# Kernel tuning notes

Measured on AMD Instinct MI355X. Metric: run time of the kernel, lower is better.

## Reference

```python
import jax, jax.numpy as jnp
import numpy as np

# Model dims
B, S, H, NH = 2, 2048, 1024, 8
HD = H // NH            # head_dim = 128
T = S * NH              # MoE input tokens per batch = 16384
E, K, F = 8, 2, 512     # experts, top_k, expert FFN dim (4*head_dim)


def setup_inputs() -> dict:
    key = jax.random.key(0)
    ks = jax.random.split(key, 9)
    s = 0.02  # init scale
    return {
        "x": jax.random.normal(ks[0], (B, S, H), jnp.float32),
        "W_mh": jax.random.normal(ks[1], (H, H), jnp.float32) * s,
        "b_mh": jnp.zeros((H,), jnp.float32),
        "W_merge": jax.random.normal(ks[2], (H, H), jnp.float32) * s,
        "b_merge": jnp.zeros((H,), jnp.float32),
        "W_router": jax.random.normal(ks[3], (HD, E), jnp.float32) * s,
        "W1": jax.random.normal(ks[4], (E, HD, F), jnp.float32) * s,
        "b1": jnp.zeros((E, F), jnp.float32),
        "W2": jax.random.normal(ks[5], (E, F, HD), jnp.float32) * s,
        "b2": jnp.zeros((E, HD), jnp.float32),
    }


def reference(x, W_mh, b_mh, W_merge, b_merge, W_router, W1, b1, W2, b2):
    # multi-head projection then split heads into the token axis
    h = x @ W_mh + b_mh                       # [B, S, H]
    h = h.reshape(B, T, HD)                   # [B, T, HD]

    # nested VectorizedMoE: top-k token-choice routing over head_dim tokens
    logits = h @ W_router                     # [B, T, E]
    probs = jax.nn.softmax(logits, axis=-1)
    topv, topi = jax.lax.top_k(probs, K)      # [B, T, K]
    topv = topv / jnp.sum(topv, axis=-1, keepdims=True)  # renormalize top-k gates
    # scatter top-k gates into dense [B, T, E] combine weights
    gates = jnp.sum(jax.nn.one_hot(topi, E, dtype=h.dtype) * topv[..., None], axis=-2)

    # vectorized expert FFNs (all experts, combined with sparse gates)
    a = jax.nn.gelu(jnp.einsum('btd,edf->btef', h, W1) + b1)   # [B, T, E, F]
    y = jnp.einsum('btef,efd->bted', a, W2) + b2               # [B, T, E, HD]
    moe_out = jnp.einsum('bte,bted->btd', gates, y)            # [B, T, HD]

    # merge heads back and final projection
    out = moe_out.reshape(B, S, H) @ W_merge + b_merge         # [B, S, H]
    return out
```

## Files before the change

kernel.cpp:

```cpp
#include <hip/hip_runtime.h>


typedef __attribute__((ext_vector_type(8))) short bf16x8;
typedef __attribute__((ext_vector_type(4))) float f32x4;
typedef __attribute__((ext_vector_type(16))) float f32x16;
typedef __attribute__((ext_vector_type(4))) unsigned short u16x4;

constexpr int NSLOT = 66560;
constexpr int NTILE_MAX = 520;
#define CTRL_CNT 0
#define CTRL_CUR 8

__device__ __forceinline__ unsigned short f2bf(float x) {
  unsigned int u = __float_as_uint(x);
  return (unsigned short)((u + 0x7FFFu + ((u >> 16) & 1u)) >> 16);
}
__device__ __forceinline__ float bf2f(unsigned short u) {
  return __uint_as_float(((unsigned int)u) << 16);
}
__device__ __forceinline__ void gload_lds16(const void* g, void* l) {
  __builtin_amdgcn_global_load_lds(
      (const __attribute__((address_space(1))) unsigned int*)g,
      (__attribute__((address_space(3))) unsigned int*)l, 16, 0, 0);
}

__global__ __launch_bounds__(256) void prep_all(
    const float* __restrict__ x, unsigned short* __restrict__ x_bf,
    const float* __restrict__ Wmh, unsigned short* __restrict__ Wmh_t,
    const float* __restrict__ Wmg, unsigned short* __restrict__ Wmg_t,
    const float* __restrict__ W1, const float* __restrict__ W2,
    unsigned short* __restrict__ W1F, unsigned short* __restrict__ W2F,
    const float* __restrict__ bmh, const float* __restrict__ Wr,
    float* __restrict__ Wc, int* __restrict__ ctrl) {
  __shared__ float smem[2048];
  const int bid = blockIdx.x, tid = threadIdx.x;
  if (bid < 1024) {
    if (bid == 0 && tid < 16) ctrl[tid] = 0;
    int i = bid * 256 + tid;
    const int n4 = 4096 * 1024 / 4, stride = 1024 * 256;
    for (; i < n4; i += stride) {
      float4 v = ((const float4*)x)[i];
      u16x4 o;
      o.x = f2bf(v.x); o.y = f2bf(v.y); o.z = f2bf(v.z); o.w = f2bf(v.w);
      ((u16x4*)x_bf)[i] = o;
    }
  } else if (bid < 3072) {
    const int b = bid - 1024;
    const float* src = (b < 1024) ? Wmh : Wmg;
    unsigned short* dst = (b < 1024) ? Wmh_t : Wmg_t;
    const int bb = b & 1023;
    const int c0 = (bb & 31) * 32, r0 = (bb >> 5) * 32;
    const int tx = tid & 31, ty = tid >> 5;
    float (*tile)[33] = (float(*)[33])smem;
    for (int i = ty; i < 32; i += 8)
      tile[i][tx] = src[(size_t)(r0 + i) * 1024 + c0 + tx];
    __syncthreads();
    for (int i = ty; i < 32; i += 8)
      dst[(size_t)(c0 + i) * 1024 + r0 + tx] = f2bf(tile[tx][i]);
  } else if (bid < 3584) {
    const int jid = (bid - 3072) * 4 + (tid >> 6);
    const int l = tid & 63;
    const int is2 = jid >= 1024;
    const int bj = is2 ? jid - 1024 : jid;
    const float* src;
    int C;
    if (!is2) {
      int kk = bj & 7, ft = (bj >> 3) & 15, e = bj >> 7;
      src = W1 + (size_t)e * 65536 + (size_t)(kk * 16) * 512 + ft * 32;
      C = 512;
    } else {
      int sht = bj & 7, ft = (bj >> 3) & 15, e = bj >> 7;
      src = W2 + (size_t)e * 65536 + (size_t)(ft * 32 + (sht >> 2) * 16) * 128 + (sht & 3) * 32;
      C = 128;
    }
    float* tile = smem + (tid >> 6) * 512;
#pragma unroll
    for (int r = 0; r < 8; ++r) {
      int i = l + 64 * r;
      tile[(i >> 5) * 32 + (i & 31)] = src[(size_t)(i >> 5) * C + (i & 31)];
    }
    __syncthreads();
    int l31 = l & 31, lh = l >> 5;
    bf16x8 v;
#pragma unroll
    for (int j = 0; j < 8; ++j) v[j] = (short)f2bf(tile[(lh * 8 + j) * 32 + l31]);
    unsigned short* dst = is2 ? W2F : W1F;
    *(bf16x8*)(dst + ((size_t)bj * 64 + l) * 8) = v;
  } else {
    const int r = (bid - 3584) * 4 + (tid >> 6);
    if (r > 1024) return;
    const int l = tid & 63;
    const float* src = (r < 1024) ? (Wmh + (size_t)r * 1024) : bmh;
    int nh = l >> 3, e = l & 7;
    float acc = 0.f;
    for (int d = 0; d < 128; ++d) acc = fmaf(src[nh * 128 + d], Wr[d * 8 + e], acc);
    Wc[(size_t)r * 64 + l] = acc;
  }
}

__global__ __launch_bounds__(256) void router_kernel(
    const float* __restrict__ x, const float* __restrict__ Wc,
    int* __restrict__ tok_e, float* __restrict__ tok_g,
    int* __restrict__ ctrl, int* __restrict__ perm, float* __restrict__ gateb) {
  int gi = blockIdx.x * 256 + threadIdx.x;
  if (gi < NSLOT) { perm[gi] = 0; gateb[gi] = 0.f; }

  __shared__ float xs[8 * 1024];
  __shared__ float lg[8][64];
  __shared__ int lcnt[8];
  if (threadIdx.x < 8) lcnt[threadIdx.x] = 0;
  int r0 = blockIdx.x * 8;
  const float4* xg = (const float4*)(x + (size_t)r0 * 1024);
  float4* xs4 = (float4*)xs;
  for (int i = threadIdx.x; i < 2048; i += 256) xs4[i] = xg[i];
  __syncthreads();
  int g = threadIdx.x >> 6, lane = threadIdx.x & 63;
  float a0 = Wc[1024 * 64 + lane], a1 = a0;
  const float* x0 = xs + g * 1024;
  const float* x1 = xs + (g + 4) * 1024;
  for (int k = 0; k < 1024; ++k) {
    float w = Wc[(size_t)k * 64 + lane];
    a0 = fmaf(x0[k], w, a0);
    a1 = fmaf(x1[k], w, a1);
  }
  lg[g][lane] = a0; lg[g + 4][lane] = a1;
  __syncthreads();
  if (threadIdx.x < 64) {
    int row = threadIdx.x >> 3, nh = threadIdx.x & 7;
    float l[8];
#pragma unroll
    for (int e = 0; e < 8; ++e) l[e] = lg[row][nh * 8 + e];
    int i1 = 0; float v1 = l[0];
#pragma unroll
    for (int e = 1; e < 8; ++e) if (l[e] > v1) { v1 = l[e]; i1 = e; }
    int i2 = -1; float v2 = -1e30f;
#pragma unroll
    for (int e = 0; e < 8; ++e) if (e != i1 && l[e] > v2) { v2 = l[e]; i2 = e; }
    float g1 = 1.f / (1.f + __expf(v2 - v1));
    float g2 = 1.f - g1;
    size_t t = (size_t)(r0 + row) * 8 + nh;
    tok_e[t * 2] = i1; tok_e[t * 2 + 1] = i2;
    tok_g[t * 2] = g1; tok_g[t * 2 + 1] = g2;
    atomicAdd(&lcnt[i1], 1);
    atomicAdd(&lcnt[i2], 1);
  }
  __syncthreads();
  if (threadIdx.x < 8 && lcnt[threadIdx.x])
    atomicAdd(&ctrl[CTRL_CNT + threadIdx.x], lcnt[threadIdx.x]);
}

__global__ __launch_bounds__(256) void assign_kernel(
    const int* __restrict__ tok_e, const float* __restrict__ tok_g,
    int* __restrict__ ctrl, int* __restrict__ perm,
    float* __restrict__ gateb, int* __restrict__ tok_slot) {
  __shared__ int lcnt[8], lbase[8];
  if (threadIdx.x < 8) lcnt[threadIdx.x] = 0;
  __syncthreads();
  int t = blockIdx.x * 256 + threadIdx.x;
  int e0 = tok_e[t * 2], e1 = tok_e[t * 2 + 1];
  int p0 = atomicAdd(&lcnt[e0], 1);
  int p1 = atomicAdd(&lcnt[e1], 1);
  __syncthreads();
  if (threadIdx.x < 8)
    lbase[threadIdx.x] = atomicAdd(&ctrl[CTRL_CUR + threadIdx.x], lcnt[threadIdx.x]);
  __syncthreads();
  int off0 = 0, off1 = 0, acc = 0;
#pragma unroll
  for (int i = 0; i < 8; ++i) {
    int cnt = ctrl[CTRL_CNT + i];
    if (i == e0) off0 = acc;
    if (i == e1) off1 = acc;
    acc += (cnt + 127) & ~127;
  }
  int s0 = off0 + lbase[e0] + p0;
  int s1 = off1 + lbase[e1] + p1;
  perm[s0] = t; perm[s1] = t;
  gateb[s0] = tok_g[t * 2]; gateb[s1] = tok_g[t * 2 + 1];
  tok_slot[t * 2] = s0; tok_slot[t * 2 + 1] = s1;
}

template <int OUT_BF16, int A_GATHER>
__global__ __launch_bounds__(256) void gemm_bt(
    const unsigned short* __restrict__ A, const unsigned short* __restrict__ Bt,
    const float* __restrict__ bias, void* __restrict__ Cout,
    int M, int N, int K,
    const unsigned short* __restrict__ ybuf, const int* __restrict__ tok_slot) {
  __shared__ unsigned short As[2][64 * 64];
  __shared__ unsigned short Bs[2][128 * 64];
  const int tid = threadIdx.x, lane = tid & 63, wid = tid >> 6;
  const int wr = wid & 1, wc = wid >> 1;
  const int m0 = blockIdx.x * 64, n0 = blockIdx.y * 128;
  const int l15 = lane & 15, lhi = lane >> 4;

  f32x4 acc[2][4];
#pragma unroll
  for (int n = 0; n < 4; ++n) {
    float bv = bias[n0 + wc * 64 + n * 16 + l15];
#pragma unroll
    for (int m = 0; m < 2; ++m) acc[m][n] = (f32x4){bv, bv, bv, bv};
  }

  const int rowi = tid >> 3;
  const int segi = (tid & 7) * 8;
  const int NT = K >> 6;

  auto stage = [&](int buf, int kt) {
    const int k0 = kt * 64;
    if constexpr (A_GATHER) {
#pragma unroll
      for (int r = 0; r < 2; ++r) {
        int arow = m0 + r * 32 + rowi;
        int k = k0 + segi;
        int tok = arow * 8 + (k >> 7);
        int hd = k & 127;
        int s0 = tok_slot[tok * 2], s1 = tok_slot[tok * 2 + 1];
        bf16x8 va = *(const bf16x8*)(ybuf + (size_t)s0 * 128 + hd);
        bf16x8 vb = *(const bf16x8*)(ybuf + (size_t)s1 * 128 + hd);
        bf16x8 vs;
#pragma unroll
        for (int j = 0; j < 8; ++j)
          vs[j] = (short)f2bf(bf2f((unsigned short)va[j]) + bf2f((unsigned short)vb[j]));
        *(bf16x8*)&As[buf][r * 2048 + tid * 8] = vs;
      }
    } else {
#pragma unroll
      for (int r = 0; r < 2; ++r)
        gload_lds16(A + (size_t)(m0 + r * 32 + rowi) * K + k0 + segi,
                    &As[buf][r * 2048 + wid * 512]);
    }
#pragma unroll
    for (int r = 0; r < 4; ++r)
      gload_lds16(Bt + (size_t)(n0 + r * 32 + rowi) * K + k0 + segi,
                  &Bs[buf][r * 2048 + wid * 512]);
  };

  stage(0, 0);
  asm volatile("s_waitcnt vmcnt(0)" ::: "memory");
  __syncthreads();
  int cur = 0;
  for (int t = 0; t < NT; ++t) {
    if (t + 1 < NT) stage(cur ^ 1, t + 1);
#pragma unroll
    for (int ks = 0; ks < 64; ks += 32) {
      bf16x8 af[2], bb[4];
#pragma unroll
      for (int m = 0; m < 2; ++m)
        af[m] = *(const bf16x8*)&As[cur][(wr * 32 + m * 16 + l15) * 64 + ks + lhi * 8];
#pragma unroll
      for (int n = 0; n < 4; ++n)
        bb[n] = *(const bf16x8*)&Bs[cur][(wc * 64 + n * 16 + l15) * 64 + ks + lhi * 8];
#pragma unroll
      for (int m = 0; m < 2; ++m)
#pragma unroll
        for (int n = 0; n < 4; ++n)
          acc[m][n] = __builtin_amdgcn_mfma_f32_16x16x32_bf16(af[m], bb[n], acc[m][n], 0, 0, 0);
    }
    asm volatile("s_waitcnt vmcnt(0)" ::: "memory");
    __syncthreads();
    cur ^= 1;
  }
#pragma unroll
  for (int m = 0; m < 2; ++m) {
#pragma unroll
    for (int n = 0; n < 4; ++n) {
      int col = n0 + wc * 64 + n * 16 + l15;
#pragma unroll
      for (int j = 0; j < 4; ++j) {
        int row = m0 + wr * 32 + m * 16 + lhi * 4 + j;
        if (OUT_BF16)
          ((unsigned short*)Cout)[(size_t)row * N + col] = f2bf(acc[m][n][j]);
        else
          ((float*)Cout)[(size_t)row * N + col] = acc[m][n][j];
      }
    }
  }
}

__global__ __launch_bounds__(256, 3) void ffn_sparse_v8(
    const unsigned short* __restrict__ hbf,
    const int* __restrict__ ctrl,
    const int* __restrict__ perm,
    const float* __restrict__ gateb,
    const unsigned short* __restrict__ W1F,
    const float* __restrict__ b1,
    const unsigned short* __restrict__ W2F,
    const float* __restrict__ b2,
    unsigned short* __restrict__ ybuf) {
  int e = -1, slotbase = 0;
  {
    int accT = 0, accS = 0;
#pragma unroll
    for (int i = 0; i < 8; ++i) {
      int cnt = ctrl[CTRL_CNT + i];
      int tiles = (cnt + 127) >> 7;
      if (e < 0 && (int)blockIdx.x < accT + tiles) {
        e = i;
        slotbase = accS + ((int)blockIdx.x - accT) * 128;
      }
      accT += tiles;
      accS += tiles * 128;
    }
  }
  if (e < 0) return;

  __shared__ __align__(16) unsigned short W1s[3][4096];
  __shared__ __align__(16) unsigned short W2s[3][4096];

  const int tid = threadIdx.x, l = tid & 63, w = tid >> 6;
  const int l31 = l & 31, lh = l >> 5;
  const int slot = slotbase + w * 32 + l31;
  const int prow = perm[slot];
  const float gate = gateb[slot];

  bf16x8 hreg[8];
  {
    const unsigned short* hsrc = hbf + (size_t)prow * 128 + lh * 8;
#pragma unroll
    for (int kk = 0; kk < 8; ++kk)
      hreg[kk] = *(const bf16x8*)(hsrc + kk * 16);
  }

  const unsigned short* W1e = W1F + (size_t)e * 65536;
  const unsigned short* W2e = W2F + (size_t)e * 65536;
  const float4* b14 = (const float4*)(b1 + (size_t)e * 512);

  auto stage = [&](int buf, int ft) {
#pragma unroll
    for (int r = 0; r < 2; ++r) {
      gload_lds16(W1e + (size_t)ft * 4096 + (size_t)(r * 256 + tid) * 8,
                  &W1s[buf][r * 2048 + w * 512]);
      gload_lds16(W2e + (size_t)ft * 4096 + (size_t)(r * 256 + tid) * 8,
                  &W2s[buf][r * 2048 + w * 512]);
    }
  };

  stage(0, 0);
  stage(1, 1);
  asm volatile("s_waitcnt vmcnt(4)" ::: "memory");
  __builtin_amdgcn_s_barrier();

  f32x16 yacc[4] = {};
  for (int it = 0; it < 16; ++it) {
    const int buf = it % 3;
    if (it + 2 < 16) stage((it + 2) % 3, it + 2);
    float4 q0 = b14[it * 8 + lh],     q1 = b14[it * 8 + lh + 2];
    float4 q2 = b14[it * 8 + lh + 4], q3 = b14[it * 8 + lh + 6];
    f32x16 accA = {q0.x, q0.y, q0.z, q0.w, q1.x, q1.y, q1.z, q1.w,
                   q2.x, q2.y, q2.z, q2.w, q3.x, q3.y, q3.z, q3.w};
    f32x16 accB = {};
    __builtin_amdgcn_s_setprio(1);
#pragma unroll
    for (int kk = 0; kk < 4; ++kk) {
      bf16x8 wA = *(const bf16x8*)&W1s[buf][(kk * 64 + l) * 8];
      bf16x8 wB = *(const bf16x8*)&W1s[buf][((kk + 4) * 64 + l) * 8];
      accA = __builtin_amdgcn_mfma_f32_32x32x16_bf16(wA, hreg[kk], accA, 0, 0, 0);
      accB = __builtin_amdgcn_mfma_f32_32x32x16_bf16(wB, hreg[kk + 4], accB, 0, 0, 0);
    }
    __builtin_amdgcn_s_setprio(0);
    f32x16 aacc = accA + accB;
    float ge[16];
#pragma unroll
    for (int r = 0; r < 16; ++r) {
      float v = aacc[r];
      float s2 = v * v;
      float q = fmaf(0.1029432f, s2, 2.3022078f);
      float E = exp2f(v * q);
      float rc = __builtin_amdgcn_rcpf(E + 1.f);
      ge[r] = fmaf(-v, rc, v);
    }
    unsigned pk[8];
#pragma unroll
    for (int p = 0; p < 8; ++p) {
      unsigned r;
      asm("v_cvt_pk_bf16_f32 %0, %1, %2" : "=v"(r) : "v"(ge[2 * p]), "v"(ge[2 * p + 1]));
      pk[p] = r;
    }
    asm volatile("v_permlane32_swap_b32 %0, %1" : "+v"(pk[0]), "+v"(pk[2]));
    asm volatile("v_permlane32_swap_b32 %0, %1" : "+v"(pk[1]), "+v"(pk[3]));
    asm volatile("v_permlane32_swap_b32 %0, %1" : "+v"(pk[4]), "+v"(pk[6]));
    asm volatile("v_permlane32_swap_b32 %0, %1" : "+v"(pk[5]), "+v"(pk[7]));
    typedef __attribute__((ext_vector_type(4))) unsigned u32x4;
    u32x4 f0 = {pk[0], pk[1], pk[2], pk[3]};
    u32x4 f1 = {pk[4], pk[5], pk[6], pk[7]};
    bf16x8 act0 = __builtin_bit_cast(bf16x8, f0);
    bf16x8 act1 = __builtin_bit_cast(bf16x8, f1);
    __builtin_amdgcn_s_setprio(1);
#pragma unroll
    for (int ht = 0; ht < 4; ++ht) {
      bf16x8 a20 = *(const bf16x8*)&W2s[buf][(ht * 64 + l) * 8];
      yacc[ht] = __builtin_amdgcn_mfma_f32_32x32x16_bf16(a20, act0, yacc[ht], 0, 0, 0);
      bf16x8 a21 = *(const bf16x8*)&W2s[buf][((4 + ht) * 64 + l) * 8];
      yacc[ht] = __builtin_amdgcn_mfma_f32_32x32x16_bf16(a21, act1, yacc[ht], 0, 0, 0);
    }
    __builtin_amdgcn_s_setprio(0);
    if (it < 15) {
      if (it + 2 < 16) {
        asm volatile("s_waitcnt vmcnt(4)" ::: "memory");
      } else {
        asm volatile("s_waitcnt vmcnt(0)" ::: "memory");
      }
      __builtin_amdgcn_s_barrier();
    }
  }
  const float* b2e = b2 + (size_t)e * 128;
#pragma unroll
  for (int ht = 0; ht < 4; ++ht) {
#pragma unroll
    for (int rp = 0; rp < 8; ++rp) {
      int fr = ((2 * rp) & 3) + 8 * (rp >> 1) + 4 * lh;
      int hd = ht * 32 + fr;
      float2 bb2 = *(const float2*)&b2e[hd];
      float v0 = gate * (yacc[ht][2 * rp] + bb2.x);
      float v1 = gate * (yacc[ht][2 * rp + 1] + bb2.y);
      unsigned pw;
      asm("v_cvt_pk_bf16_f32 %0, %1, %2" : "=v"(pw) : "v"(v0), "v"(v1));
      *(unsigned*)(ybuf + (size_t)slot * 128 + hd) = pw;
    }
  }
}

extern "C" void kernel_launch(void* const* d_in, const int* in_sizes, int n_in,
                              void* d_out, int out_size, void* d_ws, size_t ws_size,
                              hipStream_t stream) {
  const float* x       = (const float*)d_in[0];
  const float* W_mh    = (const float*)d_in[1];
  const float* b_mh    = (const float*)d_in[2];
  const float* W_merge = (const float*)d_in[3];
  const float* b_merge = (const float*)d_in[4];
  const float* W_rout  = (const float*)d_in[5];
  const float* W1      = (const float*)d_in[6];
  const float* b1      = (const float*)d_in[7];
  const float* W2      = (const float*)d_in[8];
  const float* b2      = (const float*)d_in[9];
  float* out = (float*)d_out;

  char* ws = (char*)d_ws;
  size_t off = 0;
  auto alloc = [&](size_t bytes) {
    void* p = ws + off;
    off = (off + bytes + 255) & ~(size_t)255;
    return p;
  };
  unsigned short* x_bf  = (unsigned short*)alloc((size_t)4096 * 1024 * 2);
  unsigned short* Wmh_t = (unsigned short*)alloc((size_t)1024 * 1024 * 2);
  unsigned short* Wmg_t = (unsigned short*)alloc((size_t)1024 * 1024 * 2);
  unsigned short* W1F   = (unsigned short*)alloc((size_t)8 * 512 * 128 * 2);
  unsigned short* W2F   = (unsigned short*)alloc((size_t)8 * 512 * 128 * 2);
  unsigned short* h_bf  = (unsigned short*)alloc((size_t)4096 * 1024 * 2);
  unsigned short* ybuf  = (unsigned short*)alloc((size_t)NSLOT * 128 * 2);
  float* Wc             = (float*)alloc((size_t)1025 * 64 * 4);
  int*   ctrl           = (int*)alloc(4096);
  int*   tok_e          = (int*)alloc((size_t)32768 * 2 * 4);
  float* tok_g          = (float*)alloc((size_t)32768 * 2 * 4);
  int*   tok_slot       = (int*)alloc((size_t)32768 * 2 * 4);
  int*   perm           = (int*)alloc((size_t)NSLOT * 4);
  float* gateb          = (float*)alloc((size_t)NSLOT * 4);

  prep_all<<<3841, 256, 0, stream>>>(x, x_bf, W_mh, Wmh_t, W_merge, Wmg_t,
                                     W1, W2, W1F, W2F, b_mh, W_rout, Wc, ctrl);
  router_kernel<<<512, 256, 0, stream>>>(x, Wc, tok_e, tok_g, ctrl, perm, gateb);
  assign_kernel<<<128, 256, 0, stream>>>(tok_e, tok_g, ctrl, perm, gateb, tok_slot);
  gemm_bt<1, 0><<<dim3(64, 8), 256, 0, stream>>>(x_bf, Wmh_t, b_mh, (void*)h_bf,
                                                 4096, 1024, 1024, nullptr, nullptr);
  ffn_sparse_v8<<<NTILE_MAX, 256, 0, stream>>>(h_bf, ctrl, perm, gateb, W1F, b1, W2F, b2, ybuf);
  gemm_bt<0, 1><<<dim3(64, 8), 256, 0, stream>>>(nullptr, Wmg_t, b_merge, (void*)out,
                                                 4096, 1024, 1024, ybuf, tok_slot);
}
```

Baseline: 163.3 us.

## Fuse x bf16 cast into router, enlarge GEMM tiles, simplify FFN pipeline

Moves the x-to-bf16 conversion out of the prep kernel into the router kernel, which already reads x, so x is read from memory once. The projection GEMMs switch to 128x128 tiles with 512 threads and half as many blocks. The sparse FFN kernel goes from a triple-buffered, setprio-tuned pipeline back to double buffering with full barriers, caches the biases in LDS and folds the gate into the GELU output. The combined changes risk lower occupancy and a less overlapped FFN pipeline.

Result: no change. 160.9 us (-1.5%).

```diff
diff --git a/kernel.cpp b/kernel.cpp
--- a/kernel.cpp
+++ b/kernel.cpp
@@ -25,7 +25,6 @@
 }
 
 __global__ __launch_bounds__(256) void prep_all(
-    const float* __restrict__ x, unsigned short* __restrict__ x_bf,
     const float* __restrict__ Wmh, unsigned short* __restrict__ Wmh_t,
     const float* __restrict__ Wmg, unsigned short* __restrict__ Wmg_t,
     const float* __restrict__ W1, const float* __restrict__ W2,
@@ -34,21 +33,11 @@
     float* __restrict__ Wc, int* __restrict__ ctrl) {
   __shared__ float smem[2048];
   const int bid = blockIdx.x, tid = threadIdx.x;
-  if (bid < 1024) {
+  if (bid < 2048) {
     if (bid == 0 && tid < 16) ctrl[tid] = 0;
-    int i = bid * 256 + tid;
-    const int n4 = 4096 * 1024 / 4, stride = 1024 * 256;
-    for (; i < n4; i += stride) {
-      float4 v = ((const float4*)x)[i];
-      u16x4 o;
-      o.x = f2bf(v.x); o.y = f2bf(v.y); o.z = f2bf(v.z); o.w = f2bf(v.w);
-      ((u16x4*)x_bf)[i] = o;
-    }
-  } else if (bid < 3072) {
-    const int b = bid - 1024;
-    const float* src = (b < 1024) ? Wmh : Wmg;
-    unsigned short* dst = (b < 1024) ? Wmh_t : Wmg_t;
-    const int bb = b & 1023;
+    const float* src = (bid < 1024) ? Wmh : Wmg;
+    unsigned short* dst = (bid < 1024) ? Wmh_t : Wmg_t;
+    const int bb = bid & 1023;
     const int c0 = (bb & 31) * 32, r0 = (bb >> 5) * 32;
     const int tx = tid & 31, ty = tid >> 5;
     float (*tile)[33] = (float(*)[33])smem;
@@ -57,8 +46,8 @@
     __syncthreads();
     for (int i = ty; i < 32; i += 8)
       dst[(size_t)(c0 + i) * 1024 + r0 + tx] = f2bf(tile[tx][i]);
-  } else if (bid < 3584) {
-    const int jid = (bid - 3072) * 4 + (tid >> 6);
+  } else if (bid < 2560) {
+    const int jid = (bid - 2048) * 4 + (tid >> 6);
     const int l = tid & 63;
     const int is2 = jid >= 1024;
     const int bj = is2 ? jid - 1024 : jid;
@@ -87,7 +76,7 @@
     unsigned short* dst = is2 ? W2F : W1F;
     *(bf16x8*)(dst + ((size_t)bj * 64 + l) * 8) = v;
   } else {
-    const int r = (bid - 3584) * 4 + (tid >> 6);
+    const int r = (bid - 2560) * 4 + (tid >> 6);
     if (r > 1024) return;
     const int l = tid & 63;
     const float* src = (r < 1024) ? (Wmh + (size_t)r * 1024) : bmh;
@@ -101,7 +90,8 @@
 __global__ __launch_bounds__(256) void router_kernel(
     const float* __restrict__ x, const float* __restrict__ Wc,
     int* __restrict__ tok_e, float* __restrict__ tok_g,
-    int* __restrict__ ctrl, int* __restrict__ perm, float* __restrict__ gateb) {
+    int* __restrict__ ctrl, int* __restrict__ perm, float* __restrict__ gateb,
+    unsigned short* __restrict__ x_bf) {
   int gi = blockIdx.x * 256 + threadIdx.x;
   if (gi < NSLOT) { perm[gi] = 0; gateb[gi] = 0.f; }
 
@@ -111,8 +101,15 @@
   if (threadIdx.x < 8) lcnt[threadIdx.x] = 0;
   int r0 = blockIdx.x * 8;
   const float4* xg = (const float4*)(x + (size_t)r0 * 1024);
+  u16x4* xb4 = (u16x4*)(x_bf + (size_t)r0 * 1024);
   float4* xs4 = (float4*)xs;
-  for (int i = threadIdx.x; i < 2048; i += 256) xs4[i] = xg[i];
+  for (int i = threadIdx.x; i < 2048; i += 256) {
+    float4 v = xg[i];
+    xs4[i] = v;
+    u16x4 o;
+    o.x = f2bf(v.x); o.y = f2bf(v.y); o.z = f2bf(v.z); o.w = f2bf(v.w);
+    xb4[i] = o;
+  }
   __syncthreads();
   int g = threadIdx.x >> 6, lane = threadIdx.x & 63;
   float a0 = Wc[1024 * 64 + lane], a1 = a0;
@@ -180,16 +177,16 @@
 }
 
 template <int OUT_BF16, int A_GATHER>
-__global__ __launch_bounds__(256) void gemm_bt(
+__global__ __launch_bounds__(512, 4) void gemm_bt(
     const unsigned short* __restrict__ A, const unsigned short* __restrict__ Bt,
     const float* __restrict__ bias, void* __restrict__ Cout,
     int M, int N, int K,
     const unsigned short* __restrict__ ybuf, const int* __restrict__ tok_slot) {
-  __shared__ unsigned short As[2][64 * 64];
-  __shared__ unsigned short Bs[2][128 * 64];
-  const int tid = threadIdx.x, lane = tid & 63, wid = tid >> 6;
-  const int wr = wid & 1, wc = wid >> 1;
-  const int m0 = blockIdx.x * 64, n0 = blockIdx.y * 128;
+  __shared__ __align__(16) unsigned short As[2][128 * 64];
+  __shared__ __align__(16) unsigned short Bs[2][128 * 64];
+  const int tid = threadIdx.x, lane = tid & 63, w = tid >> 6;
+  const int wr = w >> 1, wc = w & 1;
+  const int m0 = blockIdx.x * 128, n0 = blockIdx.y * 128;
   const int l15 = lane & 15, lhi = lane >> 4;
 
   f32x4 acc[2][4];
@@ -209,7 +206,7 @@
     if constexpr (A_GATHER) {
 #pragma unroll
       for (int r = 0; r < 2; ++r) {
-        int arow = m0 + r * 32 + rowi;
+        int arow = m0 + r * 64 + rowi;
         int k = k0 + segi;
         int tok = arow * 8 + (k >> 7);
         int hd = k & 127;
@@ -220,18 +217,18 @@
 #pragma unroll
         for (int j = 0; j < 8; ++j)
           vs[j] = (short)f2bf(bf2f((unsigned short)va[j]) + bf2f((unsigned short)vb[j]));
-        *(bf16x8*)&As[buf][r * 2048 + tid * 8] = vs;
+        *(bf16x8*)&As[buf][r * 4096 + tid * 8] = vs;
       }
     } else {
 #pragma unroll
       for (int r = 0; r < 2; ++r)
-        gload_lds16(A + (size_t)(m0 + r * 32 + rowi) * K + k0 + segi,
-                    &As[buf][r * 2048 + wid * 512]);
-    }
-#pragma unroll
-    for (int r = 0; r < 4; ++r)
-      gload_lds16(Bt + (size_t)(n0 + r * 32 + rowi) * K + k0 + segi,
-                  &Bs[buf][r * 2048 + wid * 512]);
+        gload_lds16(A + (size_t)(m0 + r * 64 + rowi) * K + k0 + segi,
+                    &As[buf][r * 4096 + w * 512]);
+    }
+#pragma unroll
+    for (int r = 0; r < 2; ++r)
+      gload_lds16(Bt + (size_t)(n0 + r * 64 + rowi) * K + k0 + segi,
+                  &Bs[buf][r * 4096 + w * 512]);
   };
 
   stage(0, 0);
@@ -276,7 +273,7 @@
   }
 }
 
-__global__ __launch_bounds__(256, 3) void ffn_sparse_v8(
+__global__ __launch_bounds__(256, 2) void ffn_sparse_v3(
     const unsigned short* __restrict__ hbf,
     const int* __restrict__ ctrl,
     const int* __restrict__ perm,
@@ -286,78 +283,68 @@
     const unsigned short* __restrict__ W2F,
     const float* __restrict__ b2,
     unsigned short* __restrict__ ybuf) {
-  int e = -1, slotbase = 0;
+  int e = -1;
   {
-    int accT = 0, accS = 0;
+    int accT = 0;
 #pragma unroll
     for (int i = 0; i < 8; ++i) {
-      int cnt = ctrl[CTRL_CNT + i];
-      int tiles = (cnt + 127) >> 7;
-      if (e < 0 && (int)blockIdx.x < accT + tiles) {
-        e = i;
-        slotbase = accS + ((int)blockIdx.x - accT) * 128;
-      }
+      int tiles = (ctrl[CTRL_CNT + i] + 127) >> 7;
+      if (e < 0 && (int)blockIdx.x < accT + tiles) e = i;
       accT += tiles;
-      accS += tiles * 128;
     }
   }
   if (e < 0) return;
-
-  __shared__ __align__(16) unsigned short W1s[3][4096];
-  __shared__ __align__(16) unsigned short W2s[3][4096];
-
+  __shared__ unsigned short W1c[2][4096];
+  __shared__ unsigned short W2c[2][4096];
+  __shared__ float b1_s[512];
+  __shared__ float b2_s[128];
   const int tid = threadIdx.x, l = tid & 63, w = tid >> 6;
   const int l31 = l & 31, lh = l >> 5;
-  const int slot = slotbase + w * 32 + l31;
+  const int slot = blockIdx.x * 128 + w * 32 + l31;
   const int prow = perm[slot];
   const float gate = gateb[slot];
 
   bf16x8 hreg[8];
-  {
-    const unsigned short* hsrc = hbf + (size_t)prow * 128 + lh * 8;
-#pragma unroll
-    for (int kk = 0; kk < 8; ++kk)
-      hreg[kk] = *(const bf16x8*)(hsrc + kk * 16);
-  }
+  const unsigned short* hsrc = hbf + (size_t)prow * 128 + lh * 8;
+#pragma unroll
+  for (int kk = 0; kk < 8; ++kk)
+    hreg[kk] = *(const bf16x8*)(hsrc + kk * 16);
+
+  if (tid < 128) ((float4*)b1_s)[tid] = ((const float4*)(b1 + e * 512))[tid];
+  if (tid < 32)  ((float4*)b2_s)[tid] = ((const float4*)(b2 + e * 128))[tid];
 
   const unsigned short* W1e = W1F + (size_t)e * 65536;
   const unsigned short* W2e = W2F + (size_t)e * 65536;
-  const float4* b14 = (const float4*)(b1 + (size_t)e * 512);
-
   auto stage = [&](int buf, int ft) {
 #pragma unroll
     for (int r = 0; r < 2; ++r) {
       gload_lds16(W1e + (size_t)ft * 4096 + (size_t)(r * 256 + tid) * 8,
-                  &W1s[buf][r * 2048 + w * 512]);
+                  &W1c[buf][r * 2048 + w * 512]);
       gload_lds16(W2e + (size_t)ft * 4096 + (size_t)(r * 256 + tid) * 8,
-                  &W2s[buf][r * 2048 + w * 512]);
+                  &W2c[buf][r * 2048 + w * 512]);
     }
   };
 
   stage(0, 0);
-  stage(1, 1);
-  asm volatile("s_waitcnt vmcnt(4)" ::: "memory");
-  __builtin_amdgcn_s_barrier();
+  asm volatile("s_waitcnt vmcnt(0)" ::: "memory");
+  __syncthreads();
 
   f32x16 yacc[4] = {};
-  for (int it = 0; it < 16; ++it) {
-    const int buf = it % 3;
-    if (it + 2 < 16) stage((it + 2) % 3, it + 2);
-    float4 q0 = b14[it * 8 + lh],     q1 = b14[it * 8 + lh + 2];
-    float4 q2 = b14[it * 8 + lh + 4], q3 = b14[it * 8 + lh + 6];
-    f32x16 accA = {q0.x, q0.y, q0.z, q0.w, q1.x, q1.y, q1.z, q1.w,
+  int cur = 0;
+  for (int ft = 0; ft < 16; ++ft) {
+    if (ft < 15) stage(cur ^ 1, ft + 1);
+    const float4* b14 = (const float4*)b1_s;
+    float4 q0 = b14[ft * 8 + lh];
+    float4 q1 = b14[ft * 8 + lh + 2];
+    float4 q2 = b14[ft * 8 + lh + 4];
+    float4 q3 = b14[ft * 8 + lh + 6];
+    f32x16 aacc = {q0.x, q0.y, q0.z, q0.w, q1.x, q1.y, q1.z, q1.w,
                    q2.x, q2.y, q2.z, q2.w, q3.x, q3.y, q3.z, q3.w};
-    f32x16 accB = {};
-    __builtin_amdgcn_s_setprio(1);
-#pragma unroll
-    for (int kk = 0; kk < 4; ++kk) {
-      bf16x8 wA = *(const bf16x8*)&W1s[buf][(kk * 64 + l) * 8];
-      bf16x8 wB = *(const bf16x8*)&W1s[buf][((kk + 4) * 64 + l) * 8];
-      accA = __builtin_amdgcn_mfma_f32_32x32x16_bf16(wA, hreg[kk], accA, 0, 0, 0);
-      accB = __builtin_amdgcn_mfma_f32_32x32x16_bf16(wB, hreg[kk + 4], accB, 0, 0, 0);
-    }
-    __builtin_amdgcn_s_setprio(0);
-    f32x16 aacc = accA + accB;
+#pragma unroll
+    for (int kk = 0; kk < 8; ++kk) {
+      bf16x8 a1 = *(const bf16x8*)&W1c[cur][(kk * 64 + l) * 8];
+      aacc = __builtin_amdgcn_mfma_f32_32x32x16_bf16(a1, hreg[kk], aacc, 0, 0, 0);
+    }
     float ge[16];
 #pragma unroll
     for (int r = 0; r < 16; ++r) {
@@ -366,7 +353,7 @@
       float q = fmaf(0.1029432f, s2, 2.3022078f);
       float E = exp2f(v * q);
       float rc = __builtin_amdgcn_rcpf(E + 1.f);
-      ge[r] = fmaf(-v, rc, v);
+      ge[r] = fmaf(-v, rc, v) * gate;
     }
     unsigned pk[8];
 #pragma unroll
@@ -384,34 +371,26 @@
     u32x4 f1 = {pk[4], pk[5], pk[6], pk[7]};
     bf16x8 act0 = __builtin_bit_cast(bf16x8, f0);
     bf16x8 act1 = __builtin_bit_cast(bf16x8, f1);
-    __builtin_amdgcn_s_setprio(1);
 #pragma unroll
     for (int ht = 0; ht < 4; ++ht) {
-      bf16x8 a20 = *(const bf16x8*)&W2s[buf][(ht * 64 + l) * 8];
+      bf16x8 a20 = *(const bf16x8*)&W2c[cur][(ht * 64 + l) * 8];
       yacc[ht] = __builtin_amdgcn_mfma_f32_32x32x16_bf16(a20, act0, yacc[ht], 0, 0, 0);
-      bf16x8 a21 = *(const bf16x8*)&W2s[buf][((4 + ht) * 64 + l) * 8];
+      bf16x8 a21 = *(const bf16x8*)&W2c[cur][((4 + ht) * 64 + l) * 8];
       yacc[ht] = __builtin_amdgcn_mfma_f32_32x32x16_bf16(a21, act1, yacc[ht], 0, 0, 0);
     }
-    __builtin_amdgcn_s_setprio(0);
-    if (it < 15) {
-      if (it + 2 < 16) {
-        asm volatile("s_waitcnt vmcnt(4)" ::: "memory");
-      } else {
-        asm volatile("s_waitcnt vmcnt(0)" ::: "memory");
-      }
-      __builtin_amdgcn_s_barrier();
-    }
-  }
-  const float* b2e = b2 + (size_t)e * 128;
+    asm volatile("s_waitcnt vmcnt(0)" ::: "memory");
+    __syncthreads();
+    cur ^= 1;
+  }
 #pragma unroll
   for (int ht = 0; ht < 4; ++ht) {
 #pragma unroll
     for (int rp = 0; rp < 8; ++rp) {
       int fr = ((2 * rp) & 3) + 8 * (rp >> 1) + 4 * lh;
       int hd = ht * 32 + fr;
-      float2 bb2 = *(const float2*)&b2e[hd];
-      float v0 = gate * (yacc[ht][2 * rp] + bb2.x);
-      float v1 = gate * (yacc[ht][2 * rp + 1] + bb2.y);
+      float2 bb2 = *(const float2*)&b2_s[hd];
+      float v0 = fmaf(gate, bb2.x, yacc[ht][2 * rp]);
+      float v1 = fmaf(gate, bb2.y, yacc[ht][2 * rp + 1]);
       unsigned pw;
       asm("v_cvt_pk_bf16_f32 %0, %1, %2" : "=v"(pw) : "v"(v0), "v"(v1));
       *(unsigned*)(ybuf + (size_t)slot * 128 + hd) = pw;
@@ -456,13 +435,13 @@
   int*   perm           = (int*)alloc((size_t)NSLOT * 4);
   float* gateb          = (float*)alloc((size_t)NSLOT * 4);
 
-  prep_all<<<3841, 256, 0, stream>>>(x, x_bf, W_mh, Wmh_t, W_merge, Wmg_t,
+  prep_all<<<2817, 256, 0, stream>>>(W_mh, Wmh_t, W_merge, Wmg_t,
                                      W1, W2, W1F, W2F, b_mh, W_rout, Wc, ctrl);
-  router_kernel<<<512, 256, 0, stream>>>(x, Wc, tok_e, tok_g, ctrl, perm, gateb);
+  router_kernel<<<512, 256, 0, stream>>>(x, Wc, tok_e, tok_g, ctrl, perm, gateb, x_bf);
   assign_kernel<<<128, 256, 0, stream>>>(tok_e, tok_g, ctrl, perm, gateb, tok_slot);
-  gemm_bt<1, 0><<<dim3(64, 8), 256, 0, stream>>>(x_bf, Wmh_t, b_mh, (void*)h_bf,
+  gemm_bt<1, 0><<<dim3(32, 8), 512, 0, stream>>>(x_bf, Wmh_t, b_mh, (void*)h_bf,
                                                  4096, 1024, 1024, nullptr, nullptr);
-  ffn_sparse_v8<<<NTILE_MAX, 256, 0, stream>>>(h_bf, ctrl, perm, gateb, W1F, b1, W2F, b2, ybuf);
-  gemm_bt<0, 1><<<dim3(64, 8), 256, 0, stream>>>(nullptr, Wmg_t, b_merge, (void*)out,
+  ffn_sparse_v3<<<NTILE_MAX, 256, 0, stream>>>(h_bf, ctrl, perm, gateb, W1F, b1, W2F, b2, ybuf);
+  gemm_bt<0, 1><<<dim3(32, 8), 512, 0, stream>>>(nullptr, Wmg_t, b_merge, (void*)out,
                                                  4096, 1024, 1024, ybuf, tok_slot);
 }
```
